# Kernel tuning notes

Measured on AMD Instinct MI355X. Metric: run time of the kernel, lower is better.

Reference implementation:

```python
import jax, jax.numpy as jnp
import numpy as np

B, T, N, D, R, K, P = 4, 336, 862, 64, 8, 6, 96


def setup_inputs() -> dict:
    key = jax.random.key(0)
    ks = jax.random.split(key, 8)
    s = 0.02
    return {
        "x_enc": jax.random.normal(ks[0], (B, T, N), jnp.float32),
        "W_embed": jax.random.normal(ks[1], (1, D), jnp.float32) * s,
        "b_embed": jnp.zeros((D,), jnp.float32),
        "W1": jax.random.normal(ks[2], (D, R), jnp.float32) * s,
        "W2": jax.random.normal(ks[3], (D, R), jnp.float32) * s,
        "gate": jnp.float32(-4.0),  # gate_init
        "A_prior": jnp.eye(N, dtype=jnp.float32),  # season_gcn_adj_source=identity
        "W_gcn": jax.random.normal(ks[4], (D, D), jnp.float32) * s,
        "g_gcn": jnp.float32(0.5),  # season_gcn gate
        "W_head": jax.random.normal(ks[5], (T * D, P), jnp.float32) * s,
        "b_head": jnp.zeros((P,), jnp.float32),
    }


def _topk_renorm(adj, k):
    # keep top-k entries per row, zero the rest, renormalize rows (matches _sparsify_adj)
    vals = jax.lax.top_k(adj, k)[0]
    thresh = vals[..., -1:]
    mask = (adj >= thresh).astype(adj.dtype)
    masked = adj * mask
    denom = jnp.clip(jnp.sum(masked, axis=-1, keepdims=True), 1e-12, None)
    return masked / denom


def reference(x_enc, W_embed, b_embed, W1, W2, gate, A_prior, W_gcn, g_gcn, W_head, b_head):
    # per-variable, per-timestep value embedding: [B,N,T,D]
    h = x_enc.transpose(0, 2, 1)[..., None] * W_embed[0] + b_embed
    # content-mean node descriptors: [B,N,D]
    z = jnp.mean(h, axis=2)
    # low-rank graph learner -> adjacency logits [B,N,N]
    e1 = z @ W1
    e2 = z @ W2
    logits = jnp.einsum('bnr,bmr->bnm', e1, e2) / jnp.sqrt(jnp.float32(R))
    adj = jax.nn.softmax(logits, axis=-1)
    adj = _topk_renorm(adj, K)  # top-k sparsify + row renorm
    # gated graph mixing over variable nodes
    h_mix = jnp.einsum('bnm,bmtd->bntd', adj, h)
    h = h + jax.nn.sigmoid(gate) * h_mix
    # season GCN: sym-normalized prior adjacency, residual + gate
    deg = jnp.sum(A_prior, axis=-1)
    dinv = jnp.where(deg > 0, 1.0 / jnp.sqrt(deg), 0.0)
    A_hat = A_prior * dinv[:, None] * dinv[None, :]
    h = h + g_gcn * jnp.einsum('nm,bmtd,de->bnte', A_hat, h, W_gcn)
    # forecast head: flatten tokens, project to pred_len per variable
    out = h.reshape(B, N, T * D) @ W_head + b_head  # [B,N,P]
    return out.transpose(0, 2, 1)  # [B,P,N]
```

## Files before the change

kernel.cpp:

```cpp
#include <hip/hip_runtime.h>
#include <math.h>

#define B_ 4
#define T_ 336
#define N_ 862
#define D_ 64
#define R_ 8
#define K_ 6
#define P_ 96
#define NR 896
#define CAP 32
#define NB 864

#define OFF_PCQ  0
#define OFF_XBP  768
#define OFF_DINV 21504
#define OFF_WGT  22368
#define OFF_IDX  43104
#define OFF_CNT  63840
#define OFF_CSRV 64704
#define OFF_CSRI 92352
#define OFF_P12  120000
#define OFF_PCP  184512
#define OFF_XPT  249024

__global__ __launch_bounds__(192) void kA_prep(const float* __restrict__ x,
                                               const float* __restrict__ Whead,
                                               const float* __restrict__ A,
                                               const float* __restrict__ We,
                                               const float* __restrict__ be,
                                               const float* __restrict__ gate,
                                               const float* __restrict__ Wgcn,
                                               float* __restrict__ ws) {
  int id = blockIdx.x;
  int tid = threadIdx.x;
  if (id < 336) {
    __shared__ float sW1[64], sW2[64], sCB[64], sWe[64];
    int t = id;
    float g = 1.f / (1.f + expf(-gate[0]));
    if (tid < 64) {
      float a = 0.f;
#pragma unroll
      for (int dd = 0; dd < D_; ++dd) a += We[dd] * Wgcn[dd * D_ + tid];
      sW1[tid] = a;
    } else if (tid < 128) {
      int e = tid - 64;
      float a = 0.f;
#pragma unroll
      for (int dd = 0; dd < D_; ++dd) a += be[dd] * Wgcn[dd * D_ + e];
      sW2[e] = (1.f + g) * a;
    } else {
      int e = tid - 128;
      sCB[e] = (1.f + g) * be[e];
      sWe[e] = We[e];
    }
    __syncthreads();
    int c = tid, p = c % P_, sel = c / P_;
    const float* cA = sel ? sW1 : sWe;
    const float* cB = sel ? sW2 : sCB;
    const float* wrow = Whead + (size_t)t * D_ * P_ + p;
    float a = 0.f, bacc = 0.f;
#pragma unroll
    for (int e = 0; e < D_; ++e) {
      float w = wrow[(size_t)e * P_];
      a = fmaf(cA[e], w, a);
      bacc = fmaf(cB[e], w, bacc);
    }
    ws[OFF_P12 + t * 192 + c] = a;
    ws[OFF_PCP + t * 192 + c] = bacc;
  } else if (id < 672) {
    __shared__ float part[192];
    int iq = id - 336;
    int b = iq / 84, rem = iq % 84;
    int ch = rem / 6, tg = rem % 6;
    int lane = tid & 63, tsub = tid >> 6;
    int n = ch * 64 + lane;
    float s = 0.f;
    if (n < N_) {
      const float* xp = x + (size_t)(b * T_) * N_ + n;
      int tend = tg * 56 + 56;
#pragma unroll 4
      for (int t = tg * 56 + tsub; t < tend; t += 3) s += xp[(size_t)t * N_];
    }
    part[tid] = s;
    __syncthreads();
    if (tsub == 0 && n < N_)
      ws[OFF_XBP + (size_t)(b * 6 + tg) * NB + n] =
          part[lane] + part[64 + lane] + part[128 + lane];
  } else {
    int lane = tid & 63, wv = tid >> 6;
    int n = (id - 672) * 3 + wv;
    if (n >= N_) return;
    const float* ap = A + (size_t)n * N_;
    float* vout = ws + OFF_CSRV;
    int* iout = (int*)(ws + OFF_CSRI);
    float s = 0.f;
    int total = 0;
    for (int base = 0; base < N_; base += 64) {
      int m = base + lane;
      float a = (m < N_) ? ap[m] : 0.f;
      s += a;
      bool nz = (a != 0.f);
      unsigned long long mask = __ballot(nz);
      int pos = __popcll(mask & ((1ull << lane) - 1ull));
      if (nz) {
        int slot = total + pos;
        if (slot < CAP) { vout[slot * NB + n] = a; iout[slot * NB + n] = m; }
      }
      total += __popcll(mask);
    }
    for (int off = 32; off; off >>= 1) s += __shfl_down(s, off);
    if (lane == 0) {
      ws[OFF_DINV + n] = (s > 0.f) ? (1.f / sqrtf(s)) : 0.f;
      ((int*)(ws + OFF_CNT))[n] = (total <= CAP) ? total : -1;
    }
  }
}

__global__ __launch_bounds__(192) void kM_mid(const float* __restrict__ x,
                                              const float* __restrict__ W1,
                                              const float* __restrict__ W2,
                                              const float* __restrict__ We,
                                              const float* __restrict__ be,
                                              const float* __restrict__ gate,
                                              float* __restrict__ ws) {
  __shared__ float smem[9984];
  int id = blockIdx.x;
  int tid = threadIdx.x;
  if (id < 216) {
    float* xs = smem;
    float* ps = smem + 768;
    int b = id / 54;
    int n0 = (id % 54) * 16;
    int cq = tid % 48, nq = tid / 48;
    int c0 = cq * 4;
    const float* P = ws + OFF_P12;
    float acc[4][4];
#pragma unroll
    for (int i = 0; i < 4; ++i)
#pragma unroll
      for (int j = 0; j < 4; ++j) acc[i][j] = 0.f;
    int xrow = tid >> 2, xcol4 = tid & 3;
    for (int kc = 0; kc < 7; ++kc) {
      int t0 = kc * 48;
      {
        const float* xr = x + (size_t)(b * T_ + t0 + xrow) * N_;
        if (n0 + 15 < N_) {
          *(float4*)(xs + xrow * 16 + xcol4 * 4) = *(const float4*)(xr + n0 + xcol4 * 4);
        } else {
          float* dst = xs + xrow * 16 + xcol4 * 4;
#pragma unroll
          for (int q = 0; q < 4; ++q) {
            int nn = n0 + xcol4 * 4 + q; if (nn > N_ - 1) nn = N_ - 1;
            dst[q] = xr[nn];
          }
        }
      }
#pragma unroll
      for (int sIdx = 0; sIdx < 12; ++sIdx) {
        int i4 = tid + sIdx * 192;
        int row = i4 / 48, col4 = i4 % 48;
        *(float4*)(ps + row * 192 + col4 * 4) =
            *(const float4*)(P + (size_t)(t0 + row) * 192 + col4 * 4);
      }
      __syncthreads();
#pragma unroll 4
      for (int kk = 0; kk < 48; ++kk) {
        float4 xv = *(const float4*)(xs + kk * 16 + nq * 4);
        float4 pv = *(const float4*)(ps + kk * 192 + c0);
        acc[0][0] = fmaf(pv.x, xv.x, acc[0][0]); acc[0][1] = fmaf(pv.x, xv.y, acc[0][1]);
        acc[0][2] = fmaf(pv.x, xv.z, acc[0][2]); acc[0][3] = fmaf(pv.x, xv.w, acc[0][3]);
        acc[1][0] = fmaf(pv.y, xv.x, acc[1][0]); acc[1][1] = fmaf(pv.y, xv.y, acc[1][1]);
        acc[1][2] = fmaf(pv.y, xv.z, acc[1][2]); acc[1][3] = fmaf(pv.y, xv.w, acc[1][3]);
        acc[2][0] = fmaf(pv.z, xv.x, acc[2][0]); acc[2][1] = fmaf(pv.z, xv.y, acc[2][1]);
        acc[2][2] = fmaf(pv.z, xv.z, acc[2][2]); acc[2][3] = fmaf(pv.z, xv.w, acc[2][3]);
        acc[3][0] = fmaf(pv.w, xv.x, acc[3][0]); acc[3][1] = fmaf(pv.w, xv.y, acc[3][1]);
        acc[3][2] = fmaf(pv.w, xv.z, acc[3][2]); acc[3][3] = fmaf(pv.w, xv.w, acc[3][3]);
      }
      __syncthreads();
    }
#pragma unroll
    for (int cc = 0; cc < 4; ++cc) {
      float4 v;
      v.x = acc[cc][0]; v.y = acc[cc][1]; v.z = acc[cc][2]; v.w = acc[cc][3];
      *(float4*)(ws + OFF_XPT + ((size_t)(b * 192 + c0 + cc)) * NR + n0 + nq * 4) = v;
    }
  } else if (id < 220) {
    __shared__ float s_sc[4][R_];
    __shared__ float s_scal[5];
    __shared__ float selv[12];
    __shared__ int seli[12];
    float* sx = smem;
    float* wkmax = smem + 864;
    float* wkmin = smem + 1728;
    int b = id - 216;
    if (tid < 16) {
      int r = tid & 7, which = tid >> 3;
      const float* W = which ? W2 : W1;
      float a = 0.f, bb = 0.f;
      for (int dd = 0; dd < D_; ++dd) {
        float w = W[dd * R_ + r];
        a += We[dd] * w; bb += be[dd] * w;
      }
      s_sc[which * 2][r] = a; s_sc[which * 2 + 1][r] = bb;
    }
    const float invT = 1.f / (float)T_;
    for (int i = tid; i < NB; i += 192) {
      float v = 0.f;
      if (i < N_) {
        const float* xp = ws + OFF_XBP + (size_t)(b * 6) * NB + i;
#pragma unroll
        for (int q = 0; q < 6; ++q) v += xp[q * NB];
        v *= invT;
      }
      sx[i] = v;
      wkmax[i] = (i < N_) ? v : -3.4e38f;
      wkmin[i] = (i < N_) ? v : 3.4e38f;
    }
    __syncthreads();
    if (tid == 0) {
      float s11 = 0.f, s12 = 0.f, s21 = 0.f, s22 = 0.f;
      for (int r = 0; r < R_; ++r) {
        s11 += s_sc[0][r] * s_sc[2][r];
        s12 += s_sc[0][r] * s_sc[3][r];
        s21 += s_sc[1][r] * s_sc[2][r];
        s22 += s_sc[1][r] * s_sc[3][r];
      }
      s_scal[0] = s11; s_scal[1] = s12; s_scal[2] = s21; s_scal[3] = s22;
      s_scal[4] = 1.f / (1.f + expf(-gate[0]));
    }
    if (tid < 64) {
      int lane = tid;
      for (int r = 0; r < K_; ++r) {
        float bv = -3.4e38f; int bi = 0;
        for (int i = lane; i < N_; i += 64) {
          float v = wkmax[i];
          if (v > bv) { bv = v; bi = i; }
        }
        for (int off = 32; off; off >>= 1) {
          float ov = __shfl_down(bv, off);
          int oi = __shfl_down(bi, off);
          if (ov > bv) { bv = ov; bi = oi; }
        }
        bv = __shfl(bv, 0); bi = __shfl(bi, 0);
        if (lane == 0) { selv[r] = bv; seli[r] = bi; wkmax[bi] = -3.4e38f; }
      }
    } else if (tid < 128) {
      int lane = tid - 64;
      for (int r = 0; r < K_; ++r) {
        float bv = 3.4e38f; int bi = 0;
        for (int i = lane; i < N_; i += 64) {
          float v = wkmin[i];
          if (v < bv) { bv = v; bi = i; }
        }
        for (int off = 32; off; off >>= 1) {
          float ov = __shfl_down(bv, off);
          int oi = __shfl_down(bi, off);
          if (ov < bv) { bv = ov; bi = oi; }
        }
        bv = __shfl(bv, 0); bi = __shfl(bi, 0);
        if (lane == 0) { selv[6 + r] = bv; seli[6 + r] = bi; wkmin[bi] = 3.4e38f; }
      }
    }
    __syncthreads();
    float s11 = s_scal[0], s12 = s_scal[1], s21 = s_scal[2], s22 = s_scal[3];
    float g = s_scal[4];
    const float rsq = 0.3535533906f;
    for (int n = tid; n < N_; n += 192) {
      float xn = sx[n];
      float alpha = (xn * s11 + s21) * rsq;
      float beta  = (xn * s12 + s22) * rsq;
      int base = (alpha >= 0.f) ? 0 : 6;
      float l[K_]; float mx = -3.4e38f;
#pragma unroll
      for (int j = 0; j < K_; ++j) { l[j] = alpha * selv[base + j] + beta; mx = fmaxf(mx, l[j]); }
      float e[K_]; float ss = 0.f;
#pragma unroll
      for (int j = 0; j < K_; ++j) { e[j] = expf(l[j] - mx); ss += e[j]; }
      float sc = g / ss;
#pragma unroll
      for (int j = 0; j < K_; ++j) {
        ws[OFF_WGT + j * (4 * NB) + b * NB + n] = e[j] * sc;
        ((int*)(ws + OFF_IDX))[j * (4 * NB) + b * NB + n] = seli[base + j];
      }
    }
  } else {
    int q = id - 220;
    int c = tid;
    float s = 0.f;
#pragma unroll 12
    for (int t = q * 84; t < q * 84 + 84; ++t) s += ws[OFF_PCP + t * 192 + c];
    ws[OFF_PCQ + q * 192 + c] = s;
  }
}

__global__ void kF_final(const float* __restrict__ A, const float* __restrict__ bhead,
                         const float* __restrict__ ggcn, const float* __restrict__ ws,
                         float* __restrict__ out) {
  int c = blockIdx.y;
  int n = blockIdx.x * 256 + threadIdx.x;
  if (n >= N_) return;
  int b = c / P_, p = c % P_;
  const float* Xp1 = ws + OFF_XPT + ((size_t)(b * 192 + p)) * NR;
  const float* Xp2 = ws + OFF_XPT + ((size_t)(b * 192 + P_ + p)) * NR;
  const float* WGTb = ws + OFF_WGT + b * NB;
  const int* IDXb = (const int*)(ws + OFF_IDX) + b * NB;
  float gg = ggcn[0];
  float PCp = 0.f, PAp = 0.f;
#pragma unroll
  for (int q = 0; q < 4; ++q) {
    PCp += ws[OFF_PCQ + q * 192 + p];
    PAp += ws[OFF_PCQ + q * 192 + 96 + p];
  }
  float acc1 = Xp1[n];
#pragma unroll
  for (int j = 0; j < K_; ++j)
    acc1 += WGTb[j * (4 * NB) + n] * Xp1[IDXb[j * (4 * NB) + n]];
  int cnt = ((const int*)(ws + OFF_CNT))[n];
  float S = 0.f;
  if (cnt >= 0) {
    const float* vv = ws + OFF_CSRV;
    const int* ii = (const int*)(ws + OFF_CSRI);
    for (int jj = 0; jj < cnt; ++jj) {
      float a = vv[jj * NB + n];
      int m = ii[jj * NB + n];
      float mix2 = Xp2[m];
#pragma unroll
      for (int j = 0; j < K_; ++j)
        mix2 += WGTb[j * (4 * NB) + m] * Xp2[IDXb[j * (4 * NB) + m]];
      S += a * ws[OFF_DINV + m] * (mix2 + PAp);
    }
  } else {
    const float* ar = A + (size_t)n * N_;
    for (int m = 0; m < N_; ++m) {
      float a = ar[m];
      if (a != 0.f) {
        float mix2 = Xp2[m];
#pragma unroll
        for (int j = 0; j < K_; ++j)
          mix2 += WGTb[j * (4 * NB) + m] * Xp2[IDXb[j * (4 * NB) + m]];
        S += a * ws[OFF_DINV + m] * (mix2 + PAp);
      }
    }
  }
  out[(size_t)c * N_ + n] = acc1 + gg * ws[OFF_DINV + n] * S + PCp + bhead[p];
}

extern "C" void kernel_launch(void* const* d_in, const int* in_sizes, int n_in,
                              void* d_out, int out_size, void* d_ws, size_t ws_size,
                              hipStream_t stream) {
  const float* x     = (const float*)d_in[0];
  const float* We    = (const float*)d_in[1];
  const float* be    = (const float*)d_in[2];
  const float* W1    = (const float*)d_in[3];
  const float* W2    = (const float*)d_in[4];
  const float* gate  = (const float*)d_in[5];
  const float* A     = (const float*)d_in[6];
  const float* Wgcn  = (const float*)d_in[7];
  const float* ggcn  = (const float*)d_in[8];
  const float* Whead = (const float*)d_in[9];
  const float* bhead = (const float*)d_in[10];
  float* ws = (float*)d_ws;
  float* out = (float*)d_out;

  kA_prep<<<960, 192, 0, stream>>>(x, Whead, A, We, be, gate, Wgcn, ws);
  kM_mid<<<224, 192, 0, stream>>>(x, W1, W2, We, be, gate, ws);
  kF_final<<<dim3(4, 384), 256, 0, stream>>>(A, bhead, ggcn, ws, out);
}
```

Measured before the change: 113.1 us.

## Stage W_head in LDS, retile mid GEMM, reuse own top-k weights

kA_prep now loads each timestep's W_head slab into shared memory with float4 loads instead of strided global reads. kM_mid's x-projection GEMM is retiled to 8-node tiles with 256 threads and 3x2 register tiles, doubling block count for better occupancy at the cost of less register reuse per thread. kF_final caches its own top-k weights and indices in registers and reuses them when the CSR neighbour equals the node itself, which avoids repeated gathers for the identity-prior case.

```diff
diff --git a/kernel.cpp b/kernel.cpp
--- a/kernel.cpp
+++ b/kernel.cpp
@@ -35,8 +35,15 @@
   int id = blockIdx.x;
   int tid = threadIdx.x;
   if (id < 336) {
+    __shared__ float swh[6144];
     __shared__ float sW1[64], sW2[64], sCB[64], sWe[64];
     int t = id;
+    const float* wbase = Whead + (size_t)t * (D_ * P_);
+#pragma unroll
+    for (int s = 0; s < 8; ++s) {
+      int idx4 = s * 192 + tid;
+      *(float4*)(swh + idx4 * 4) = *(const float4*)(wbase + idx4 * 4);
+    }
     float g = 1.f / (1.f + expf(-gate[0]));
     if (tid < 64) {
       float a = 0.f;
@@ -58,11 +65,10 @@
     int c = tid, p = c % P_, sel = c / P_;
     const float* cA = sel ? sW1 : sWe;
     const float* cB = sel ? sW2 : sCB;
-    const float* wrow = Whead + (size_t)t * D_ * P_ + p;
     float a = 0.f, bacc = 0.f;
 #pragma unroll
     for (int e = 0; e < D_; ++e) {
-      float w = wrow[(size_t)e * P_];
+      float w = swh[e * P_ + p];
       a = fmaf(cA[e], w, a);
       bacc = fmaf(cB[e], w, bacc);
     }
@@ -117,75 +123,71 @@
   }
 }
 
-__global__ __launch_bounds__(192) void kM_mid(const float* __restrict__ x,
+__global__ __launch_bounds__(256) void kM_mid(const float* __restrict__ x,
                                               const float* __restrict__ W1,
                                               const float* __restrict__ W2,
                                               const float* __restrict__ We,
                                               const float* __restrict__ be,
                                               const float* __restrict__ gate,
                                               float* __restrict__ ws) {
-  __shared__ float smem[9984];
+  __shared__ float smem[9600];
   int id = blockIdx.x;
   int tid = threadIdx.x;
-  if (id < 216) {
+  if (id < 432) {
     float* xs = smem;
-    float* ps = smem + 768;
-    int b = id / 54;
-    int n0 = (id % 54) * 16;
-    int cq = tid % 48, nq = tid / 48;
-    int c0 = cq * 4;
+    float* ps = smem + 384;
+    int b = id / 108;
+    int n0 = (id % 108) * 8;
+    int cg_ = tid & 63, ng = tid >> 6;
+    int c0 = cg_ * 3;
     const float* P = ws + OFF_P12;
-    float acc[4][4];
-#pragma unroll
-    for (int i = 0; i < 4; ++i)
-#pragma unroll
-      for (int j = 0; j < 4; ++j) acc[i][j] = 0.f;
-    int xrow = tid >> 2, xcol4 = tid & 3;
+    float a00 = 0.f, a01 = 0.f, a10 = 0.f, a11 = 0.f, a20 = 0.f, a21 = 0.f;
     for (int kc = 0; kc < 7; ++kc) {
       int t0 = kc * 48;
-      {
-        const float* xr = x + (size_t)(b * T_ + t0 + xrow) * N_;
-        if (n0 + 15 < N_) {
-          *(float4*)(xs + xrow * 16 + xcol4 * 4) = *(const float4*)(xr + n0 + xcol4 * 4);
+      if (tid < 96) {
+        int row = tid >> 1, col4 = (tid & 1) * 4;
+        const float* xr = x + (size_t)(b * T_ + t0 + row) * N_;
+        if (n0 + 7 < N_) {
+          *(float4*)(xs + row * 8 + col4) = *(const float4*)(xr + n0 + col4);
         } else {
-          float* dst = xs + xrow * 16 + xcol4 * 4;
+          float* dst = xs + row * 8 + col4;
 #pragma unroll
           for (int q = 0; q < 4; ++q) {
-            int nn = n0 + xcol4 * 4 + q; if (nn > N_ - 1) nn = N_ - 1;
+            int nn = n0 + col4 + q; if (nn > N_ - 1) nn = N_ - 1;
             dst[q] = xr[nn];
           }
         }
       }
 #pragma unroll
-      for (int sIdx = 0; sIdx < 12; ++sIdx) {
-        int i4 = tid + sIdx * 192;
+      for (int sIdx = 0; sIdx < 9; ++sIdx) {
+        int i4 = tid + sIdx * 256;
         int row = i4 / 48, col4 = i4 % 48;
         *(float4*)(ps + row * 192 + col4 * 4) =
             *(const float4*)(P + (size_t)(t0 + row) * 192 + col4 * 4);
       }
       __syncthreads();
-#pragma unroll 4
+#pragma unroll 6
       for (int kk = 0; kk < 48; ++kk) {
-        float4 xv = *(const float4*)(xs + kk * 16 + nq * 4);
-        float4 pv = *(const float4*)(ps + kk * 192 + c0);
-        acc[0][0] = fmaf(pv.x, xv.x, acc[0][0]); acc[0][1] = fmaf(pv.x, xv.y, acc[0][1]);
-        acc[0][2] = fmaf(pv.x, xv.z, acc[0][2]); acc[0][3] = fmaf(pv.x, xv.w, acc[0][3]);
-        acc[1][0] = fmaf(pv.y, xv.x, acc[1][0]); acc[1][1] = fmaf(pv.y, xv.y, acc[1][1]);
-        acc[1][2] = fmaf(pv.y, xv.z, acc[1][2]); acc[1][3] = fmaf(pv.y, xv.w, acc[1][3]);
-        acc[2][0] = fmaf(pv.z, xv.x, acc[2][0]); acc[2][1] = fmaf(pv.z, xv.y, acc[2][1]);
-        acc[2][2] = fmaf(pv.z, xv.z, acc[2][2]); acc[2][3] = fmaf(pv.z, xv.w, acc[2][3]);
-        acc[3][0] = fmaf(pv.w, xv.x, acc[3][0]); acc[3][1] = fmaf(pv.w, xv.y, acc[3][1]);
-        acc[3][2] = fmaf(pv.w, xv.z, acc[3][2]); acc[3][3] = fmaf(pv.w, xv.w, acc[3][3]);
+        float x0 = xs[kk * 8 + ng * 2];
+        float x1 = xs[kk * 8 + ng * 2 + 1];
+        float p0 = ps[kk * 192 + c0];
+        float p1 = ps[kk * 192 + c0 + 1];
+        float p2 = ps[kk * 192 + c0 + 2];
+        a00 = fmaf(p0, x0, a00); a01 = fmaf(p0, x1, a01);
+        a10 = fmaf(p1, x0, a10); a11 = fmaf(p1, x1, a11);
+        a20 = fmaf(p2, x0, a20); a21 = fmaf(p2, x1, a21);
       }
       __syncthreads();
     }
-#pragma unroll
-    for (int cc = 0; cc < 4; ++cc) {
-      float4 v;
-      v.x = acc[cc][0]; v.y = acc[cc][1]; v.z = acc[cc][2]; v.w = acc[cc][3];
-      *(float4*)(ws + OFF_XPT + ((size_t)(b * 192 + c0 + cc)) * NR + n0 + nq * 4) = v;
-    }
-  } else if (id < 220) {
+    int n = n0 + ng * 2;
+    float accs[3][2] = {{a00, a01}, {a10, a11}, {a20, a21}};
+#pragma unroll
+    for (int cc = 0; cc < 3; ++cc) {
+      float* op = ws + OFF_XPT + ((size_t)(b * 192 + c0 + cc)) * NR + n;
+      if (n + 1 < N_) { *(float2*)op = *(float2*)accs[cc]; }
+      else if (n < N_) { op[0] = accs[cc][0]; }
+    }
+  } else if (id < 436) {
     __shared__ float s_sc[4][R_];
     __shared__ float s_scal[5];
     __shared__ float selv[12];
@@ -193,7 +195,7 @@
     float* sx = smem;
     float* wkmax = smem + 864;
     float* wkmin = smem + 1728;
-    int b = id - 216;
+    int b = id - 432;
     if (tid < 16) {
       int r = tid & 7, which = tid >> 3;
       const float* W = which ? W2 : W1;
@@ -205,7 +207,7 @@
       s_sc[which * 2][r] = a; s_sc[which * 2 + 1][r] = bb;
     }
     const float invT = 1.f / (float)T_;
-    for (int i = tid; i < NB; i += 192) {
+    for (int i = tid; i < NB; i += 256) {
       float v = 0.f;
       if (i < N_) {
         const float* xp = ws + OFF_XBP + (size_t)(b * 6) * NB + i;
@@ -266,7 +268,7 @@
     float s11 = s_scal[0], s12 = s_scal[1], s21 = s_scal[2], s22 = s_scal[3];
     float g = s_scal[4];
     const float rsq = 0.3535533906f;
-    for (int n = tid; n < N_; n += 192) {
+    for (int n = tid; n < N_; n += 256) {
       float xn = sx[n];
       float alpha = (xn * s11 + s21) * rsq;
       float beta  = (xn * s12 + s22) * rsq;
@@ -285,18 +287,21 @@
       }
     }
   } else {
-    int q = id - 220;
-    int c = tid;
-    float s = 0.f;
+    int q = id - 436;
+    if (tid < 192) {
+      float s = 0.f;
 #pragma unroll 12
-    for (int t = q * 84; t < q * 84 + 84; ++t) s += ws[OFF_PCP + t * 192 + c];
-    ws[OFF_PCQ + q * 192 + c] = s;
+      for (int t = q * 84; t < q * 84 + 84; ++t) s += ws[OFF_PCP + t * 192 + tid];
+      ws[OFF_PCQ + q * 192 + tid] = s;
+    }
   }
 }
 
-__global__ void kF_final(const float* __restrict__ A, const float* __restrict__ bhead,
-                         const float* __restrict__ ggcn, const float* __restrict__ ws,
-                         float* __restrict__ out) {
+__global__ __launch_bounds__(256) void kF_final(const float* __restrict__ A,
+                                                const float* __restrict__ bhead,
+                                                const float* __restrict__ ggcn,
+                                                const float* __restrict__ ws,
+                                                float* __restrict__ out) {
   int c = blockIdx.y;
   int n = blockIdx.x * 256 + threadIdx.x;
   if (n >= N_) return;
@@ -312,10 +317,15 @@
     PCp += ws[OFF_PCQ + q * 192 + p];
     PAp += ws[OFF_PCQ + q * 192 + 96 + p];
   }
+  float wj[K_]; int ij[K_];
+#pragma unroll
+  for (int j = 0; j < K_; ++j) {
+    wj[j] = WGTb[j * (4 * NB) + n];
+    ij[j] = IDXb[j * (4 * NB) + n];
+  }
   float acc1 = Xp1[n];
 #pragma unroll
-  for (int j = 0; j < K_; ++j)
-    acc1 += WGTb[j * (4 * NB) + n] * Xp1[IDXb[j * (4 * NB) + n]];
+  for (int j = 0; j < K_; ++j) acc1 += wj[j] * Xp1[ij[j]];
   int cnt = ((const int*)(ws + OFF_CNT))[n];
   float S = 0.f;
   if (cnt >= 0) {
@@ -325,9 +335,14 @@
       float a = vv[jj * NB + n];
       int m = ii[jj * NB + n];
       float mix2 = Xp2[m];
-#pragma unroll
-      for (int j = 0; j < K_; ++j)
-        mix2 += WGTb[j * (4 * NB) + m] * Xp2[IDXb[j * (4 * NB) + m]];
+      if (m == n) {
+#pragma unroll
+        for (int j = 0; j < K_; ++j) mix2 += wj[j] * Xp2[ij[j]];
+      } else {
+#pragma unroll
+        for (int j = 0; j < K_; ++j)
+          mix2 += WGTb[j * (4 * NB) + m] * Xp2[IDXb[j * (4 * NB) + m]];
+      }
       S += a * ws[OFF_DINV + m] * (mix2 + PAp);
     }
   } else {
@@ -364,6 +379,6 @@
   float* out = (float*)d_out;
 
   kA_prep<<<960, 192, 0, stream>>>(x, Whead, A, We, be, gate, Wgcn, ws);
-  kM_mid<<<224, 192, 0, stream>>>(x, W1, W2, We, be, gate, ws);
+  kM_mid<<<440, 256, 0, stream>>>(x, W1, W2, We, be, gate, ws);
   kF_final<<<dim3(4, 384), 256, 0, stream>>>(A, bhead, ggcn, ws, out);
 }
```

After: 115.4 us. 2.0% more time.
